# Performance work log

Measured on AMD Instinct MI355X. Metric: run time of the kernel, lower is better.

The kernel has to match this reference:

```python
import jax, jax.numpy as jnp
import numpy as np

HIDDEN = 2048
NH = 16
NKV = 8
HD = 128
EPS = 1e-6
THETA = 10000.0
Q_SIZE = NH * HD
KV_SIZE = NKV * HD


def setup_inputs() -> dict:
    key = jax.random.key(0)
    k1, k2, k3, k4 = jax.random.split(key, 4)
    B, T = 2, 2048
    hidden_states = jax.random.normal(k1, (B, T, HIDDEN), dtype=jnp.float32)
    positions = jnp.broadcast_to(jnp.arange(T, dtype=jnp.int32)[None, :], (B, T))
    # learned params
    w_qkv = jax.random.normal(k2, (Q_SIZE + 2 * KV_SIZE, HIDDEN), dtype=jnp.float32) * (HIDDEN ** -0.5)
    w_o = jax.random.normal(k3, (HIDDEN, Q_SIZE), dtype=jnp.float32) * (Q_SIZE ** -0.5)
    rms_w = jnp.ones((HD,), dtype=jnp.float32) + 0.01 * jax.random.normal(k4, (HD,), dtype=jnp.float32)
    return {"positions": positions, "hidden_states": hidden_states,
            "w_qkv": w_qkv, "w_o": w_o, "rms_w": rms_w}


def _rms_norm(x, w):
    # per-head RMSNorm over last dim (head_dim)
    var = jnp.mean(jnp.square(x), axis=-1, keepdims=True)
    return x * jax.lax.rsqrt(var + EPS) * w


def _rope(positions, x):
    # NeoX-style rotary over full head_dim. positions: [B,T], x: [B,T,h,HD]
    half = HD // 2
    inv_freq = 1.0 / (THETA ** (jnp.arange(0, half, dtype=jnp.float32) / half))
    angles = positions.astype(jnp.float32)[..., None] * inv_freq  # [B,T,half]
    cos = jnp.cos(angles)[:, :, None, :]  # [B,T,1,half]
    sin = jnp.sin(angles)[:, :, None, :]
    x1, x2 = jnp.split(x, 2, axis=-1)
    return jnp.concatenate([x1 * cos - x2 * sin, x2 * cos + x1 * sin], axis=-1)


def reference(positions, hidden_states, w_qkv, w_o, rms_w):
    B, T, _ = hidden_states.shape
    qkv = jnp.einsum('bth,oh->bto', hidden_states, w_qkv)
    q = qkv[..., :Q_SIZE].reshape(B, T, NH, HD)
    k = qkv[..., Q_SIZE:Q_SIZE + KV_SIZE].reshape(B, T, NKV, HD)
    v = qkv[..., Q_SIZE + KV_SIZE:].reshape(B, T, NKV, HD)
    # QK-norm (qkv_bias=False path)
    q = _rms_norm(q, rms_w)
    k = _rms_norm(k, rms_w)
    q, k = _rope(positions, q), _rope(positions, k)
    # GQA attention, causal. group q heads onto kv heads: g = NH // NKV
    g = NH // NKV
    qg = q.reshape(B, T, NKV, g, HD)
    scale = HD ** -0.5
    scores = jnp.einsum('btkgd,bskd->bkgts', qg, k) * scale  # [B,NKV,g,T,T]
    causal = jnp.tril(jnp.ones((T, T), dtype=bool))
    scores = jnp.where(causal, scores, jnp.finfo(scores.dtype).min)
    probs = jax.nn.softmax(scores, axis=-1)
    o = jnp.einsum('bkgts,bskd->btkgd', probs, v).reshape(B, T, Q_SIZE)
    return jnp.einsum('bto,ho->bth', o, w_o)
```

## Files before the change

### kernel.cpp

```cpp
#include <hip/hip_runtime.h>
#include <hip/hip_bf16.h>

typedef __attribute__((ext_vector_type(8))) short short8;
typedef __attribute__((ext_vector_type(8))) unsigned short u16x8;
typedef __attribute__((ext_vector_type(4))) float f32x4;
typedef __attribute__((ext_vector_type(16))) float f32x16;

#define HIDDEN 2048
#define NH 16
#define NKV 8
#define HD 128
#define T_SEQ 2048
#define B_SZ 2
#define M_TOK (B_SZ * T_SEQ)
#define QSIZE (NH * HD)
#define KVSIZE (NKV * HD)
#define OUTQKV (QSIZE + 2 * KVSIZE)

__device__ __forceinline__ unsigned short f2bf(float f) {
  unsigned int u = __builtin_bit_cast(unsigned int, f);
  u += 0x7FFFu + ((u >> 16) & 1u);
  return (unsigned short)(u >> 16);
}
__device__ __forceinline__ float bf2f(unsigned short h) {
  return __builtin_bit_cast(float, (unsigned int)h << 16);
}

typedef __attribute__((address_space(3))) void lds_void;
typedef __attribute__((address_space(1))) const void glb_void;
__device__ __forceinline__ void gld16(const void* g, void* l) {
  __builtin_amdgcn_global_load_lds((glb_void*)g, (lds_void*)l, 16, 0, 0);
}

__device__ __forceinline__ float exp2fast(float x) {
  float r;
  asm("v_exp_f32 %0, %1" : "=v"(r) : "v"(x));
  return r;
}
__device__ __forceinline__ unsigned cvtpk(float lo, float hi) {
  unsigned r;
  asm("v_cvt_pk_bf16_f32 %0, %1, %2" : "=v"(r) : "v"(lo), "v"(hi));
  return r;
}
__device__ __forceinline__ void pl32swap(unsigned& a, unsigned& b) {
  asm volatile("v_permlane32_swap_b32 %0, %1" : "+v"(a), "+v"(b));
}

template <int N>
__device__ __forceinline__ void vwait();
template <> __device__ __forceinline__ void vwait<0>() { asm volatile("s_waitcnt vmcnt(0)" ::: "memory"); }
template <> __device__ __forceinline__ void vwait<3>() { asm volatile("s_waitcnt vmcnt(3)" ::: "memory"); }
template <> __device__ __forceinline__ void vwait<4>() { asm volatile("s_waitcnt vmcnt(4)" ::: "memory"); }

__device__ __forceinline__ void store4(unsigned short* p, const f32x4& v) {
  ushort4 o;
  o.x = f2bf(v[0]); o.y = f2bf(v[1]); o.z = f2bf(v[2]); o.w = f2bf(v[3]);
  *(ushort4*)p = o;
}
__device__ __forceinline__ void store4(float* p, const f32x4& v) {
  float4 o = {v[0], v[1], v[2], v[3]};
  *(float4*)p = o;
}

#define SEG0 1048576
#define SEG1 1048576
#define SEG2 524288
__global__ __launch_bounds__(256) void prep_kernel(const float* __restrict__ hidden,
                                                   const float* __restrict__ w_qkv,
                                                   const float* __restrict__ w_o,
                                                   unsigned short* __restrict__ hb,
                                                   unsigned short* __restrict__ wqkvb,
                                                   unsigned short* __restrict__ wob) {
  size_t i = (size_t)blockIdx.x * blockDim.x + threadIdx.x;
  const float* src;
  unsigned short* dst;
  if (i < SEG0) { src = hidden; dst = hb; }
  else if (i < SEG0 + SEG1) { src = w_qkv; dst = wqkvb; i -= SEG0; }
  else { src = w_o; dst = wob; i -= (SEG0 + SEG1); }
  const float4* p = (const float4*)src + i * 2;
  float4 a = p[0], b = p[1];
  u16x8 o = {f2bf(a.x), f2bf(a.y), f2bf(a.z), f2bf(a.w),
             f2bf(b.x), f2bf(b.y), f2bf(b.z), f2bf(b.w)};
  ((u16x8*)dst)[i] = o;
}

template <int MT, typename TC>
__global__ __launch_bounds__(512, 2) void gemm8(const unsigned short* __restrict__ A,
                                                const unsigned short* __restrict__ B,
                                                TC* __restrict__ C,
                                                int M, int N, int K) {
  constexpr int BM = MT * 32;
  constexpr int MT2 = MT / 2;
  constexpr int VMN = (MT == 8) ? 4 : 3;
  __shared__ unsigned short lsA[4][BM * 32];
  __shared__ unsigned short lsB[4][8192];
  const int tid = threadIdx.x;
  const int wave = tid >> 6, lane = tid & 63;
  const int wr = wave >> 2, wc = wave & 3;
  const int lr = lane & 15;
  const int ntn = N >> 8;
  const int cpx = gridDim.x >> 3;
  const int wg = (blockIdx.x & 7) * cpx + (blockIdx.x >> 3);
  const int m0 = (wg / ntn) * BM, n0 = (wg % ntn) * 256;
  const int ce = 8 * ((lane >> 4) ^ ((lr >> 1) & 3));
  const int rr0 = tid >> 2;
  const int cle = 8 * ((tid & 3) ^ ((rr0 >> 1) & 3));
  const unsigned short* pA0 = A + (size_t)(m0 + rr0) * K + cle;
  const unsigned short* pA1 = pA0 + (size_t)128 * K;
  const unsigned short* pB0 = B + (size_t)(n0 + rr0) * K + cle;
  const unsigned short* pB1 = pB0 + (size_t)128 * K;
  const int dst0 = 8 * tid, dst1 = 4096 + 8 * tid;

  auto stageA = [&](int hn) {
    const int s = hn & 3;
    gld16(pA0 + hn * 32, &lsA[s][dst0]);
    if constexpr (MT == 8) gld16(pA1 + hn * 32, &lsA[s][dst1]);
  };
  auto stageB = [&](int hn) {
    const int s = hn & 3;
    gld16(pB0 + hn * 32, &lsB[s][dst0]);
    gld16(pB1 + hn * 32, &lsB[s][dst1]);
  };

  f32x4 acc[MT][4] = {};
  short8 af[MT2], bfg[4];
  const int NT = K >> 6;

  stageA(0); stageB(0); stageA(1); stageB(1);
  vwait<0>();
  __syncthreads();

#define PHASE(KK, MH, STG, VM)                                                            \
  {                                                                                       \
    const int slot = sb + (KK);                                                           \
    _Pragma("unroll")                                                                     \
    for (int i = 0; i < MT2; i++)                                                         \
      af[i] = *(const short8*)&lsA[slot][(wr * (MT * 16) + (MH) * (MT * 8) + i * 16 + lr) * 32 + ce]; \
    if ((MH) == 0) {                                                                      \
      _Pragma("unroll")                                                                   \
      for (int j = 0; j < 4; j++)                                                         \
        bfg[j] = *(const short8*)&lsB[slot][(wc * 64 + j * 16 + lr) * 32 + ce];           \
    }                                                                                     \
    if (st) { STG; }                                                                      \
    if ((VM) == 1) {                                                                      \
      if (st) vwait<VMN>(); else vwait<0>();                                              \
    } else if ((VM) == 2) {                                                               \
      if (st) vwait<VMN>();                                                               \
    }                                                                                     \
    __builtin_amdgcn_s_setprio(1);                                                        \
    _Pragma("unroll")                                                                     \
    for (int i = 0; i < MT2; i++)                                                         \
      _Pragma("unroll")                                                                   \
      for (int j = 0; j < 4; j++)                                                         \
        acc[(MH)*MT2 + i][j] =                                                            \
            __builtin_amdgcn_mfma_f32_16x16x32_bf16(bfg[j], af[i], acc[(MH)*MT2 + i][j], 0, 0, 0); \
    __builtin_amdgcn_s_setprio(0);                                                        \
    __builtin_amdgcn_s_barrier();                                                         \
  }

  for (int t = 0; t < NT; t++) {
    const int sb = (2 * t) & 3;
    const bool st = (t < NT - 1);
    const int h2 = 2 * t + 2, h3 = 2 * t + 3;
    PHASE(0, 0, stageA(h2), 0)
    PHASE(0, 1, stageB(h2), 1)
    PHASE(1, 0, stageA(h3), 0)
    PHASE(1, 1, stageB(h3), 2)
  }
#undef PHASE

#pragma unroll
  for (int i = 0; i < MT; i++)
#pragma unroll
    for (int j = 0; j < 4; j++) {
      int gm = m0 + wr * (MT * 16) + i * 16 + lr;
      int gn = n0 + wc * 64 + j * 16 + (lane >> 4) * 4;
      store4(C + (size_t)gm * N + gn, acc[i][j]);
    }
}

__global__ void norm_rope_kernel(const unsigned short* __restrict__ qkv,
                                 const int* __restrict__ positions,
                                 const float* __restrict__ rms_w,
                                 unsigned short* __restrict__ qa,
                                 unsigned short* __restrict__ ka) {
  const int m = blockIdx.x;
  const int b = m >> 11, tt = m & 2047;
  const int lane = threadIdx.x;
  const float pos = (float)positions[m];
  const float inv_freq = powf(10000.0f, -(float)lane * (1.0f / 64.0f));
  float sv, cv;
  sincosf(pos * inv_freq, &sv, &cv);
  const float w1 = rms_w[lane], w2 = rms_w[lane + 64];
  const unsigned short* src = qkv + (size_t)m * OUTQKV;
  for (int h = 0; h < 24; h++) {
    unsigned short r1 = src[h * 128 + lane], r2 = src[h * 128 + 64 + lane];
    float x1 = bf2f(r1), x2 = bf2f(r2);
    float ss = x1 * x1 + x2 * x2;
    ss += __shfl_xor(ss, 1);  ss += __shfl_xor(ss, 2);  ss += __shfl_xor(ss, 4);
    ss += __shfl_xor(ss, 8);  ss += __shfl_xor(ss, 16); ss += __shfl_xor(ss, 32);
    float rstd = rsqrtf(ss * (1.0f / 128.0f) + 1e-6f);
    float y1 = x1 * rstd * w1, y2 = x2 * rstd * w2;
    float o1 = y1 * cv - y2 * sv, o2 = y2 * cv + y1 * sv;
    unsigned short* dst;
    if (h < 16) dst = qa + (((size_t)b * NH + h) * T_SEQ + tt) * HD;
    else        dst = ka + (((size_t)b * NKV + (h - 16)) * T_SEQ + tt) * HD;
    dst[lane] = f2bf(o1); dst[lane + 64] = f2bf(o2);
  }
}

__global__ __launch_bounds__(256) void v_transpose(const unsigned short* __restrict__ qkv,
                                                   unsigned short* __restrict__ vat) {
  __shared__ unsigned short tile[64][136];
  const int tt0 = blockIdx.x * 64;
  const int kvh = blockIdx.y, b = blockIdx.z;
  const int t = threadIdx.x;
  {
    const int tok = t >> 2, d0 = (t & 3) * 32;
    const unsigned short* src = qkv + (size_t)((size_t)b * T_SEQ + tt0 + tok) * OUTQKV
                                + QSIZE + KVSIZE + kvh * HD + d0;
#pragma unroll
    for (int i = 0; i < 4; i++)
      *(u16x8*)&tile[tok][d0 + i * 8] = *(const u16x8*)(src + i * 8);
  }
  __syncthreads();
  {
    const int d = t >> 1, c0 = (t & 1) * 32;
    unsigned short* dst = vat + ((size_t)((size_t)b * NKV + kvh) * HD + d) * T_SEQ + tt0 + c0;
#pragma unroll
    for (int j = 0; j < 4; j++) {
      u16x8 v;
#pragma unroll
      for (int e = 0; e < 8; e++) v[e] = tile[c0 + j * 8 + e][d];
      *(u16x8*)(dst + j * 8) = v;
    }
  }
}

__global__ __launch_bounds__(256, 2) void attn_kernel(const unsigned short* __restrict__ qa,
                                                      const unsigned short* __restrict__ ka,
                                                      const unsigned short* __restrict__ vat,
                                                      unsigned short* __restrict__ ob) {
  __shared__ unsigned short ks[2][64 * 128];
  __shared__ unsigned short vs[2][128 * 64];
  const int bx = blockIdx.x;
  const int qt = 31 - (bx >> 4);
  const int kvh = bx & 7, b = (bx >> 3) & 1;
  const int tid = threadIdx.x, w = tid >> 6, lane = tid & 63;
  const int l31 = lane & 31, h5 = lane >> 5;
  const int h = kvh * 2 + (w >> 1);
  const int qrow = qt * 64 + (w & 1) * 32 + l31;
  const float cexp = 0.08838834764831845f * 1.44269504088896340f;

  const unsigned short* Kg = ka + ((size_t)b * NKV + kvh) * T_SEQ * HD;
  const unsigned short* Vg = vat + ((size_t)b * NKV + kvh) * (size_t)HD * T_SEQ;

  short8 qf[8];
  {
    const unsigned short* Qg = qa + (((size_t)b * NH + h) * T_SEQ + qrow) * HD;
#pragma unroll
    for (int c = 0; c < 8; c++) qf[c] = *(const short8*)(Qg + c * 16 + h5 * 8);
  }

  auto stage = [&](int j, int buf) {
#pragma unroll
    for (int s = 0; s < 4; s++) {
      int g = s * 256 + tid;
      int kr = g >> 4;
      int kc = 8 * ((g & 15) ^ (kr & 15));
      gld16(Kg + (size_t)(j * 64 + kr) * HD + kc, &ks[buf][g * 8]);
    }
#pragma unroll
    for (int s = 0; s < 4; s++) {
      int g = s * 256 + tid;
      int vd = g >> 3;
      int vc = 8 * ((g & 7) ^ (vd & 7));
      gld16(Vg + (size_t)vd * T_SEQ + j * 64 + vc, &vs[buf][g * 8]);
    }
  };

  stage(0, 0);
  vwait<0>();
  __syncthreads();

  f32x16 oacc[4] = {};
  float mraw = -1e30f, m2 = -3.0e29f, lsum = 0.f;

  for (int j = 0; j <= qt; j++) {
    const int buf = j & 1;
    if (j < qt) stage(j + 1, buf ^ 1);

    f32x16 sacc[2] = {};
    __builtin_amdgcn_s_setprio(1);
#pragma unroll
    for (int c = 0; c < 8; c++) {
#pragma unroll
      for (int t = 0; t < 2; t++) {
        const int row = t * 32 + l31;
        short8 kf = *(const short8*)&ks[buf][row * 128 + ((c * 16 + h5 * 8) ^ (8 * (l31 & 15)))];
        sacc[t] = __builtin_amdgcn_mfma_f32_32x32x16_bf16(kf, qf[c], sacc[t], 0, 0, 0);
      }
    }
    __builtin_amdgcn_s_setprio(0);

    if (j * 64 + 63 > qt * 64 + (w & 1) * 32) {
#pragma unroll
      for (int t = 0; t < 2; t++)
#pragma unroll
        for (int r = 0; r < 16; r++) {
          int kvg = j * 64 + t * 32 + (r & 3) + 8 * (r >> 2) + 4 * h5;
          if (kvg > qrow) sacc[t][r] = -1e30f;
        }
    }
    float mx = sacc[0][0];
#pragma unroll
    for (int t = 0; t < 2; t++)
#pragma unroll
      for (int r = 0; r < 16; r++) mx = fmaxf(mx, sacc[t][r]);
    mx = fmaxf(mx, __shfl_xor(mx, 32));
    if (__any((mx - mraw) * cexp > 11.5f)) {
      float mn = fmaxf(mraw, mx);
      float corr = exp2fast((mraw - mn) * cexp);
      mraw = mn;
      m2 = mn * cexp;
      lsum *= corr;
#pragma unroll
      for (int dt = 0; dt < 4; dt++)
#pragma unroll
        for (int r = 0; r < 16; r++) oacc[dt][r] *= corr;
    }
    short8 pf[4];
#pragma unroll
    for (int kt = 0; kt < 4; kt++) {
      const int t = kt >> 1, r0 = (kt & 1) * 8;
      float e0 = exp2fast(sacc[t][r0 + 0] * cexp - m2);
      float e1 = exp2fast(sacc[t][r0 + 1] * cexp - m2);
      float e2 = exp2fast(sacc[t][r0 + 2] * cexp - m2);
      float e3 = exp2fast(sacc[t][r0 + 3] * cexp - m2);
      float e4 = exp2fast(sacc[t][r0 + 4] * cexp - m2);
      float e5 = exp2fast(sacc[t][r0 + 5] * cexp - m2);
      float e6 = exp2fast(sacc[t][r0 + 6] * cexp - m2);
      float e7 = exp2fast(sacc[t][r0 + 7] * cexp - m2);
      lsum += ((e0 + e1) + (e2 + e3)) + ((e4 + e5) + (e6 + e7));
      unsigned a0 = cvtpk(e0, e1), a1 = cvtpk(e2, e3);
      unsigned b0 = cvtpk(e4, e5), b1 = cvtpk(e6, e7);
      pl32swap(a0, b0);
      pl32swap(a1, b1);
      uint4 uu = make_uint4(a0, a1, b0, b1);
      pf[kt] = __builtin_bit_cast(short8, uu);
    }
    __builtin_amdgcn_s_setprio(1);
#pragma unroll
    for (int dt = 0; dt < 4; dt++) {
      const int d = dt * 32 + l31;
#pragma unroll
      for (int kt = 0; kt < 4; kt++) {
        short8 vf = *(const short8*)&vs[buf][d * 64 + ((kt * 16 + h5 * 8) ^ (8 * (l31 & 7)))];
        oacc[dt] = __builtin_amdgcn_mfma_f32_32x32x16_bf16(vf, pf[kt], oacc[dt], 0, 0, 0);
      }
    }
    __builtin_amdgcn_s_setprio(0);
    vwait<0>();
    __syncthreads();
  }

  lsum += __shfl_xor(lsum, 32);
  const float inv = 1.0f / lsum;
  unsigned short* dst = ob + ((size_t)b * T_SEQ + qrow) * QSIZE + h * HD;
#pragma unroll
  for (int dt = 0; dt < 4; dt++)
#pragma unroll
    for (int rg = 0; rg < 4; rg++) {
      ushort4 v4;
      v4.x = f2bf(oacc[dt][rg * 4 + 0] * inv);
      v4.y = f2bf(oacc[dt][rg * 4 + 1] * inv);
      v4.z = f2bf(oacc[dt][rg * 4 + 2] * inv);
      v4.w = f2bf(oacc[dt][rg * 4 + 3] * inv);
      *(ushort4*)(dst + dt * 32 + rg * 8 + 4 * h5) = v4;
    }
}

extern "C" void kernel_launch(void* const* d_in, const int* in_sizes, int n_in,
                              void* d_out, int out_size, void* d_ws, size_t ws_size,
                              hipStream_t stream) {
  const int* positions = (const int*)d_in[0];
  const float* hidden  = (const float*)d_in[1];
  const float* w_qkv   = (const float*)d_in[2];
  const float* w_o     = (const float*)d_in[3];
  const float* rms_w   = (const float*)d_in[4];
  float* out = (float*)d_out;

  unsigned short* qkv   = (unsigned short*)d_ws;
  unsigned short* hb    = qkv + (size_t)M_TOK * OUTQKV;
  unsigned short* wqkvb = hb + (size_t)M_TOK * HIDDEN;
  unsigned short* wob   = wqkvb + (size_t)OUTQKV * HIDDEN;
  unsigned short* qa    = hb;
  unsigned short* ka    = wqkvb;
  unsigned short* vat   = wqkvb + (size_t)B_SZ * NKV * T_SEQ * HD;
  unsigned short* ob    = qkv;

  const int prep_items = SEG0 + SEG1 + SEG2;
  prep_kernel<<<prep_items / 256, 256, 0, stream>>>(hidden, w_qkv, w_o, hb, wqkvb, wob);
  gemm8<8, unsigned short>
      <<<256, 512, 0, stream>>>(hb, wqkvb, qkv, M_TOK, OUTQKV, HIDDEN);
  norm_rope_kernel<<<M_TOK, 64, 0, stream>>>(qkv, positions, rms_w, qa, ka);
  v_transpose<<<dim3(T_SEQ / 64, NKV, B_SZ), 256, 0, stream>>>(qkv, vat);
  attn_kernel<<<512, 256, 0, stream>>>(qa, ka, vat, ob);
  gemm8<4, float>
      <<<256, 512, 0, stream>>>(ob, wob, out, M_TOK, HIDDEN, QSIZE);
}
```

Before: 211.0 us.

## Replace four-stage phased GEMM pipeline with simple double-buffered K loop

The bf16 MFMA GEMM drops its 4-slot LDS ring and the four-phase macro with partial vmcnt waits and per-phase barriers. It now uses a 2-slot double buffer: each 32-wide K step loads fragments, issues the next step's global-to-LDS copies, runs two MFMA half-blocks, then does a full vmcnt wait and one block barrier. This halves LDS use, which may allow more resident blocks, and removes three barriers per step. In exchange, prefetch depth drops to one step and every iteration stalls on a full memory drain, so global latency is less well hidden.

```diff
diff --git a/kernel.cpp b/kernel.cpp
--- a/kernel.cpp
+++ b/kernel.cpp
@@ -49,8 +49,6 @@
 template <int N>
 __device__ __forceinline__ void vwait();
 template <> __device__ __forceinline__ void vwait<0>() { asm volatile("s_waitcnt vmcnt(0)" ::: "memory"); }
-template <> __device__ __forceinline__ void vwait<3>() { asm volatile("s_waitcnt vmcnt(3)" ::: "memory"); }
-template <> __device__ __forceinline__ void vwait<4>() { asm volatile("s_waitcnt vmcnt(4)" ::: "memory"); }
 
 __device__ __forceinline__ void store4(unsigned short* p, const f32x4& v) {
   ushort4 o;
@@ -91,9 +89,8 @@
                                                 int M, int N, int K) {
   constexpr int BM = MT * 32;
   constexpr int MT2 = MT / 2;
-  constexpr int VMN = (MT == 8) ? 4 : 3;
-  __shared__ unsigned short lsA[4][BM * 32];
-  __shared__ unsigned short lsB[4][8192];
+  __shared__ unsigned short lsA[2][BM * 32];
+  __shared__ unsigned short lsB[2][8192];
   const int tid = threadIdx.x;
   const int wave = tid >> 6, lane = tid & 63;
   const int wr = wave >> 2, wc = wave & 3;
@@ -111,63 +108,55 @@
   const unsigned short* pB1 = pB0 + (size_t)128 * K;
   const int dst0 = 8 * tid, dst1 = 4096 + 8 * tid;
 
-  auto stageA = [&](int hn) {
-    const int s = hn & 3;
-    gld16(pA0 + hn * 32, &lsA[s][dst0]);
-    if constexpr (MT == 8) gld16(pA1 + hn * 32, &lsA[s][dst1]);
+  auto stageA = [&](int c) {
+    const int s = c & 1;
+    gld16(pA0 + c * 32, &lsA[s][dst0]);
+    if constexpr (MT == 8) gld16(pA1 + c * 32, &lsA[s][dst1]);
   };
-  auto stageB = [&](int hn) {
-    const int s = hn & 3;
-    gld16(pB0 + hn * 32, &lsB[s][dst0]);
-    gld16(pB1 + hn * 32, &lsB[s][dst1]);
+  auto stageB = [&](int c) {
+    const int s = c & 1;
+    gld16(pB0 + c * 32, &lsB[s][dst0]);
+    gld16(pB1 + c * 32, &lsB[s][dst1]);
   };
 
   f32x4 acc[MT][4] = {};
   short8 af[MT2], bfg[4];
-  const int NT = K >> 6;
-
-  stageA(0); stageB(0); stageA(1); stageB(1);
+  const int NT = K >> 5;
+
+  stageA(0); stageB(0);
   vwait<0>();
   __syncthreads();
 
-#define PHASE(KK, MH, STG, VM)                                                            \
-  {                                                                                       \
-    const int slot = sb + (KK);                                                           \
-    _Pragma("unroll")                                                                     \
-    for (int i = 0; i < MT2; i++)                                                         \
-      af[i] = *(const short8*)&lsA[slot][(wr * (MT * 16) + (MH) * (MT * 8) + i * 16 + lr) * 32 + ce]; \
-    if ((MH) == 0) {                                                                      \
-      _Pragma("unroll")                                                                   \
-      for (int j = 0; j < 4; j++)                                                         \
-        bfg[j] = *(const short8*)&lsB[slot][(wc * 64 + j * 16 + lr) * 32 + ce];           \
-    }                                                                                     \
-    if (st) { STG; }                                                                      \
-    if ((VM) == 1) {                                                                      \
-      if (st) vwait<VMN>(); else vwait<0>();                                              \
-    } else if ((VM) == 2) {                                                               \
-      if (st) vwait<VMN>();                                                               \
-    }                                                                                     \
-    __builtin_amdgcn_s_setprio(1);                                                        \
-    _Pragma("unroll")                                                                     \
-    for (int i = 0; i < MT2; i++)                                                         \
-      _Pragma("unroll")                                                                   \
-      for (int j = 0; j < 4; j++)                                                         \
-        acc[(MH)*MT2 + i][j] =                                                            \
-            __builtin_amdgcn_mfma_f32_16x16x32_bf16(bfg[j], af[i], acc[(MH)*MT2 + i][j], 0, 0, 0); \
-    __builtin_amdgcn_s_setprio(0);                                                        \
-    __builtin_amdgcn_s_barrier();                                                         \
-  }
-
   for (int t = 0; t < NT; t++) {
-    const int sb = (2 * t) & 3;
+    const int slot = t & 1;
     const bool st = (t < NT - 1);
-    const int h2 = 2 * t + 2, h3 = 2 * t + 3;
-    PHASE(0, 0, stageA(h2), 0)
-    PHASE(0, 1, stageB(h2), 1)
-    PHASE(1, 0, stageA(h3), 0)
-    PHASE(1, 1, stageB(h3), 2)
-  }
-#undef PHASE
+#pragma unroll
+    for (int j = 0; j < 4; j++)
+      bfg[j] = *(const short8*)&lsB[slot][(wc * 64 + j * 16 + lr) * 32 + ce];
+#pragma unroll
+    for (int i = 0; i < MT2; i++)
+      af[i] = *(const short8*)&lsA[slot][(wr * (MT * 16) + i * 16 + lr) * 32 + ce];
+    if (st) { stageA(t + 1); stageB(t + 1); }
+    __builtin_amdgcn_s_setprio(1);
+#pragma unroll
+    for (int i = 0; i < MT2; i++)
+#pragma unroll
+      for (int j = 0; j < 4; j++)
+        acc[i][j] = __builtin_amdgcn_mfma_f32_16x16x32_bf16(bfg[j], af[i], acc[i][j], 0, 0, 0);
+    __builtin_amdgcn_s_setprio(0);
+#pragma unroll
+    for (int i = 0; i < MT2; i++)
+      af[i] = *(const short8*)&lsA[slot][(wr * (MT * 16) + MT * 8 + i * 16 + lr) * 32 + ce];
+    __builtin_amdgcn_s_setprio(1);
+#pragma unroll
+    for (int i = 0; i < MT2; i++)
+#pragma unroll
+      for (int j = 0; j < 4; j++)
+        acc[MT2 + i][j] = __builtin_amdgcn_mfma_f32_16x16x32_bf16(bfg[j], af[i], acc[MT2 + i][j], 0, 0, 0);
+    __builtin_amdgcn_s_setprio(0);
+    vwait<0>();
+    __syncthreads();
+  }
 
 #pragma unroll
   for (int i = 0; i < MT; i++)
```

Measured after the change: 219.2 us. 1.04x slower.
